# Optimization experiments

Hardware: AMD Instinct MI355X
Metric: run time of the kernel (lower is better)

Reference implementation:

```python
import jax, jax.numpy as jnp
import numpy as np

EPS = 1e-6
NEG_SLOPE = 0.2


def knn_idx(xf, k):
    # xf: (B, C, N) flattened vector features; returns (B, N, k) neighbor indices
    xx = jnp.sum(xf * xf, axis=1)                       # (B, N)
    inner = jnp.einsum('bcn,bcm->bnm', xf, xf)          # (B, N, N)
    neg_dist = 2.0 * inner - xx[:, :, None] - xx[:, None, :]  # -||xi-xj||^2
    _, idx = jax.lax.top_k(neg_dist, k)                 # includes self (dist 0)
    return idx


def get_graph_feature(x, k):
    # x: (B, D, 3, N) -> edge features (B, 2D, 3, N, k)
    B, D, _, N = x.shape
    idx = knn_idx(x.reshape(B, D * 3, N), k)            # (B, N, k)
    pts = jnp.transpose(x, (0, 3, 1, 2))                # (B, N, D, 3)
    neigh = jax.vmap(lambda p, i: p[i])(pts, idx)       # (B, N, k, D, 3) gather
    center = jnp.broadcast_to(pts[:, :, None], neigh.shape)
    feat = jnp.concatenate([neigh - center, center], axis=3)  # (B, N, k, 2D, 3)
    return jnp.transpose(feat, (0, 3, 4, 1, 2))


def vn_linear_leakyrelu(x, Wf, Wd):
    # Vector-Neuron linear + leaky ReLU. x: (B, Cin, 3, ...),
    # Wf: (Cout, Cin), Wd: (Cout, Cin) or (1, Cin) when nonlinearity is shared.
    p = jnp.einsum('oi,bi...->bo...', Wf, x)
    d = jnp.einsum('oi,bi...->bo...', Wd, x)
    dot = jnp.sum(p * d, axis=2, keepdims=True)
    dsq = jnp.sum(d * d, axis=2, keepdims=True)
    proj = p - (dot / (dsq + EPS)) * d
    return NEG_SLOPE * p + (1.0 - NEG_SLOPE) * jnp.where(dot >= 0, p, proj)


def setup_inputs() -> dict:
    key = jax.random.key(0)
    ks = jax.random.split(key, 11)
    B, N = 8, 1024
    x = jax.random.normal(ks[0], (B, 3, N), dtype=jnp.float32)
    # dims = [1, 21, 21, 42, 85, 341]
    ins = [2, 42, 42, 84, 169]      # 2*dim_in for edge layers; sum(dims[1:-1]) for last
    outs = [21, 21, 42, 85, 341]
    dirs = [21, 21, 42, 85, 1]      # last layer has share_nonlinearity=True
    d = {"x": x}
    for i, (ci, co, cd) in enumerate(zip(ins, outs, dirs)):
        s = 1.0 / np.sqrt(ci)
        kf, kd = jax.random.split(ks[1 + i])
        d[f"Wf{i}"] = (jax.random.normal(kf, (co, ci), dtype=jnp.float32) * s)
        d[f"Wd{i}"] = (jax.random.normal(kd, (cd, ci), dtype=jnp.float32) * s)
    d["k"] = 20
    return d


def reference(x, Wf0, Wd0, Wf1, Wd1, Wf2, Wd2, Wf3, Wd3, Wf4, Wd4, k):
    cur = x[:, None]                 # (B, 1, 3, N)
    feats = []
    for Wf, Wd in ((Wf0, Wd0), (Wf1, Wd1), (Wf2, Wd2), (Wf3, Wd3)):
        g = get_graph_feature(cur, k)        # (B, 2D, 3, N, k)
        h = vn_linear_leakyrelu(g, Wf, Wd)   # (B, Dout, 3, N, k)
        cur = h.mean(axis=-1)                # mean over neighbors -> (B, Dout, 3, N)
        feats.append(cur)
    xcat = jnp.concatenate(feats, axis=1)    # (B, 169, 3, N)
    out = vn_linear_leakyrelu(xcat, Wf4, Wd4)
    return out.mean(axis=-1)                 # mean over points -> (B, 341, 3)
```

## Files before the change

kernel.cpp:

```cpp
#include <hip/hip_runtime.h>
#include <cstddef>

#define BB 8
#define NN 1024
#define KK 20
#define CCAT 169
#define NT 16
#define WTLD 384

__global__ __launch_bounds__(256) void dist_tile_kernel(
    const float* __restrict__ src, int bs, int F, float* __restrict__ dist) {
  __shared__ float As[8][128];
  __shared__ float Bs[8][128];
  int b = blockIdx.z;
  int rem = blockIdx.x, bi = 0;
  while (rem >= 8 - bi) { rem -= 8 - bi; ++bi; }
  int bj = bi + rem;
  int n0 = bi * 128;
  int m0 = bj * 128;
  int t = threadIdx.x;
  int tx = t & 15, ty = t >> 4;
  const float* p = src + (size_t)b * bs;

  float acc[8][8];
  float xn[8], xm[8];
#pragma unroll
  for (int i = 0; i < 8; ++i) {
    xn[i] = 0.f;
    xm[i] = 0.f;
#pragma unroll
    for (int j = 0; j < 8; ++j) acc[i][j] = 0.f;
  }

  int fr = t >> 5;
  int cc = (t & 31) << 2;
  for (int f0 = 0; f0 < F; f0 += 8) {
    int f = f0 + fr;
    float4 av = {0.f, 0.f, 0.f, 0.f}, bv = {0.f, 0.f, 0.f, 0.f};
    if (f < F) {
      av = *(const float4*)(p + (size_t)f * NN + n0 + cc);
      bv = *(const float4*)(p + (size_t)f * NN + m0 + cc);
    }
    __syncthreads();
    *(float4*)&As[fr][cc] = av;
    *(float4*)&Bs[fr][cc] = bv;
    __syncthreads();
#pragma unroll
    for (int f2 = 0; f2 < 8; ++f2) {
      float4 al = *(const float4*)&As[f2][ty << 2];
      float4 ah = *(const float4*)&As[f2][64 + (ty << 2)];
      float4 bl = *(const float4*)&Bs[f2][tx << 2];
      float4 bh = *(const float4*)&Bs[f2][64 + (tx << 2)];
      float a[8] = {al.x, al.y, al.z, al.w, ah.x, ah.y, ah.z, ah.w};
      float bb[8] = {bl.x, bl.y, bl.z, bl.w, bh.x, bh.y, bh.z, bh.w};
#pragma unroll
      for (int i = 0; i < 8; ++i) xn[i] += a[i] * a[i];
#pragma unroll
      for (int j = 0; j < 8; ++j) xm[j] += bb[j] * bb[j];
#pragma unroll
      for (int i = 0; i < 8; ++i)
#pragma unroll
        for (int j = 0; j < 8; ++j) acc[i][j] += a[i] * bb[j];
    }
  }

#pragma unroll
  for (int i = 0; i < 8; ++i)
#pragma unroll
    for (int j = 0; j < 8; ++j) acc[i][j] = 2.f * acc[i][j] - xn[i] - xm[j];

#pragma unroll
  for (int i = 0; i < 8; ++i) {
    int n = n0 + ((i < 4) ? ((ty << 2) + i) : (64 + (ty << 2) + i - 4));
    float* dr = dist + (((size_t)b * NN + n) << 10);
    *(float4*)(dr + m0 + (tx << 2)) =
        make_float4(acc[i][0], acc[i][1], acc[i][2], acc[i][3]);
    *(float4*)(dr + m0 + 64 + (tx << 2)) =
        make_float4(acc[i][4], acc[i][5], acc[i][6], acc[i][7]);
  }

  if (bi != bj) {
#pragma unroll
    for (int j = 0; j < 8; ++j) {
      int m = m0 + ((j < 4) ? ((tx << 2) + j) : (64 + (tx << 2) + j - 4));
      float* dr = dist + (((size_t)b * NN + m) << 10);
      *(float4*)(dr + n0 + (ty << 2)) =
          make_float4(acc[0][j], acc[1][j], acc[2][j], acc[3][j]);
      *(float4*)(dr + n0 + 64 + (ty << 2)) =
          make_float4(acc[4][j], acc[5][j], acc[6][j], acc[7][j]);
    }
  }
}

__global__ __launch_bounds__(256) void topk_kernel(
    const float* __restrict__ dist, int* __restrict__ idx_out) {
  int wave = threadIdx.x >> 6;
  int lane = threadIdx.x & 63;
  int row = blockIdx.x * 4 + wave;
  const float* d = dist + ((size_t)row << 10);

  unsigned long long key[16];
  {
    const float4* dp = (const float4*)(d + (lane << 4));
#pragma unroll
    for (int q = 0; q < 4; ++q) {
      float4 v4 = dp[q];
      float vv[4] = {v4.x, v4.y, v4.z, v4.w};
#pragma unroll
      for (int e = 0; e < 4; ++e) {
        int m = (lane << 4) + (q << 2) + e;
        unsigned u = __float_as_uint(vv[e]);
        u = (u & 0x80000000u) ? ~u : (u | 0x80000000u);
        key[(q << 2) + e] =
            ((unsigned long long)u << 32) | (unsigned)(NN - 1 - m);
      }
    }
  }

#pragma unroll
  for (int size = 2; size <= 16; size <<= 1) {
#pragma unroll
    for (int stride = size >> 1; stride > 0; stride >>= 1) {
#pragma unroll
      for (int i = 0; i < 16; ++i) {
        int j = i ^ stride;
        if (j > i) {
          unsigned long long a = key[i], c = key[j];
          bool desc = ((i & size) == 0);
          bool sw = desc ? (a < c) : (a > c);
          key[i] = sw ? c : a;
          key[j] = sw ? a : c;
        }
      }
    }
  }

  int* out = idx_out + row * KK;
  unsigned long long head = key[0];
  for (int r = 0; r < KK; ++r) {
    unsigned hv = (unsigned)(head >> 32);
    unsigned v = hv;
#pragma unroll
    for (int off = 32; off > 0; off >>= 1) {
      unsigned o = __shfl_xor(v, off, 64);
      v = (o > v) ? o : v;
    }
    unsigned long long tie = __ballot(hv == v);
    unsigned il;
    if (tie & (tie - 1)) {
      unsigned c = (hv == v) ? (unsigned)head : 0u;
#pragma unroll
      for (int off = 32; off > 0; off >>= 1) {
        unsigned o = __shfl_xor(c, off, 64);
        c = (o > c) ? o : c;
      }
      il = c;
    } else {
      int wl = __builtin_ctzll(tie);
      il = __shfl((unsigned)head, wl, 64);
    }
    if (lane == 0) out[r] = (NN - 1) - (int)il;
    if (hv == v && (unsigned)head == il) {
#pragma unroll
      for (int s = 0; s < 15; ++s) key[s] = key[s + 1];
      key[15] = 0ull;
      head = key[0];
    }
  }
}

template <int DD>
__global__ __launch_bounds__(256) void edge_fused_kernel(
    const float* __restrict__ src, int bs, int Co, int nsplit,
    const float* __restrict__ Wf, const float* __restrict__ Wd,
    const int* __restrict__ idx, int ooff, float* __restrict__ xcat) {
  __shared__ float2 Ulds[3 * NN];
  __shared__ float2 Vlds[3 * NN];
  __shared__ float4 Wlds[48];
  int bo = blockIdx.x;
  int b = bo / Co, o = bo % Co;
  int t = threadIdx.x;

  if (t < DD) {
    float wfa = Wf[o * 2 * DD + t];
    float wfb = Wf[o * 2 * DD + DD + t] - wfa;
    float wda = Wd[o * 2 * DD + t];
    float wdb = Wd[o * 2 * DD + DD + t] - wda;
    Wlds[t] = make_float4(wfa, wfb, wda, wdb);
  }
  __syncthreads();

  const float* sb = src + (size_t)b * bs;
  {
    int c0 = t << 2;
    float4 uf[3], vf[3], ud[3], vd[3];
#pragma unroll
    for (int r = 0; r < 3; ++r) {
      uf[r] = make_float4(0.f, 0.f, 0.f, 0.f);
      vf[r] = make_float4(0.f, 0.f, 0.f, 0.f);
      ud[r] = make_float4(0.f, 0.f, 0.f, 0.f);
      vd[r] = make_float4(0.f, 0.f, 0.f, 0.f);
    }
#pragma unroll 2
    for (int i = 0; i < DD; ++i) {
      const float* row = sb + (size_t)i * 3 * NN + c0;
      float4 s[3];
      s[0] = *(const float4*)(row);
      s[1] = *(const float4*)(row + 1024);
      s[2] = *(const float4*)(row + 2048);
      float4 w = Wlds[i];
#pragma unroll
      for (int r = 0; r < 3; ++r) {
        uf[r].x += w.x * s[r].x; uf[r].y += w.x * s[r].y;
        uf[r].z += w.x * s[r].z; uf[r].w += w.x * s[r].w;
        vf[r].x += w.y * s[r].x; vf[r].y += w.y * s[r].y;
        vf[r].z += w.y * s[r].z; vf[r].w += w.y * s[r].w;
        ud[r].x += w.z * s[r].x; ud[r].y += w.z * s[r].y;
        ud[r].z += w.z * s[r].z; ud[r].w += w.z * s[r].w;
        vd[r].x += w.w * s[r].x; vd[r].y += w.w * s[r].y;
        vd[r].z += w.w * s[r].z; vd[r].w += w.w * s[r].w;
      }
    }
#pragma unroll
    for (int r = 0; r < 3; ++r) {
      int g = t + 256 * r;
      *(float4*)&Ulds[(g << 2) + 0] =
          make_float4(uf[r].x, ud[r].x, uf[r].y, ud[r].y);
      *(float4*)&Ulds[(g << 2) + 2] =
          make_float4(uf[r].z, ud[r].z, uf[r].w, ud[r].w);
      *(float4*)&Vlds[(g << 2) + 0] =
          make_float4(vf[r].x, vd[r].x, vf[r].y, vd[r].y);
      *(float4*)&Vlds[(g << 2) + 2] =
          make_float4(vf[r].z, vd[r].z, vf[r].w, vd[r].w);
    }
  }
  __syncthreads();

  const float inv_k = 1.f / KK;
  int cnt = NN / nsplit;
  int nbase = blockIdx.y * cnt;
  for (int n = nbase + t; n < nbase + cnt; n += 256) {
    float2 v0 = Vlds[n];
    float2 v1 = Vlds[NN + n];
    float2 v2 = Vlds[2 * NN + n];
    const int4* ip = (const int4*)(idx + (b * NN + n) * KK);
    float a0 = 0.f, a1 = 0.f, a2 = 0.f;
#pragma unroll
    for (int q = 0; q < 5; ++q) {
      int4 iv = ip[q];
      int nbs[4] = {iv.x, iv.y, iv.z, iv.w};
#pragma unroll
      for (int jj = 0; jj < 4; ++jj) {
        int nb = nbs[jj];
        float2 u0 = Ulds[nb];
        float2 u1 = Ulds[NN + nb];
        float2 u2 = Ulds[2 * NN + nb];
        float pf0 = u0.x + v0.x, pd0 = u0.y + v0.y;
        float pf1 = u1.x + v1.x, pd1 = u1.y + v1.y;
        float pf2 = u2.x + v2.x, pd2 = u2.y + v2.y;
        float dot = pf0 * pd0 + pf1 * pd1 + pf2 * pd2;
        float dsq = pd0 * pd0 + pd1 * pd1 + pd2 * pd2;
        float g = (dot >= 0.f) ? 0.f : 0.8f * dot / (dsq + 1e-6f);
        a0 += pf0 - g * pd0;
        a1 += pf1 - g * pd1;
        a2 += pf2 - g * pd2;
      }
    }
    size_t ob = (size_t)b * CCAT * 3 * NN + (size_t)(ooff + o) * 3 * NN + n;
    xcat[ob] = a0 * inv_k;
    xcat[ob + NN] = a1 * inv_k;
    xcat[ob + 2 * NN] = a2 * inv_k;
  }
}

__global__ __launch_bounds__(256) void prep_kernel(
    const float* __restrict__ Wf4, float* __restrict__ Wt,
    float* __restrict__ zpad) {
  int o = blockIdx.x * 256 + threadIdx.x;
  int f = blockIdx.y;
  if (o < WTLD)
    Wt[(size_t)f * WTLD + o] = (f < CCAT && o < 341) ? Wf4[o * CCAT + f] : 0.f;
  if (blockIdx.x == 0 && blockIdx.y == 0) zpad[threadIdx.x] = 0.f;
}

__device__ __forceinline__ void gl2lds16(const float* g, float* l) {
  __builtin_amdgcn_global_load_lds(
      (const __attribute__((address_space(1))) unsigned int*)g,
      (__attribute__((address_space(3))) unsigned int*)l, 16, 0, 0);
}

__global__ __launch_bounds__(256) void final_fused_kernel(
    const float* __restrict__ xcat, const float* __restrict__ Wt,
    const float* __restrict__ Wd4, const float* __restrict__ zpad,
    float* __restrict__ part) {
  __shared__ float Ws[2][16][64];
  __shared__ float Xs[2][3][16][64];
  __shared__ float Wda[176];
  int b = blockIdx.z;
  int o0 = blockIdx.y * 64;
  int n0 = blockIdx.x * 64;
  int t = threadIdx.x;
  int tx = t & 15, ty = t >> 4;

  if (t < 176) Wda[t] = (t < CCAT) ? Wd4[t] : 0.f;

  float acc[3][4][4];
  float dv[3][4];
#pragma unroll
  for (int c = 0; c < 3; ++c) {
#pragma unroll
    for (int i = 0; i < 4; ++i)
#pragma unroll
      for (int j = 0; j < 4; ++j) acc[c][i][j] = 0.f;
#pragma unroll
    for (int j = 0; j < 4; ++j) dv[c][j] = 0.f;
  }

  const float* xb = xcat + (size_t)b * CCAT * 3 * NN;
  const int NTILE = 11;

  {
    const float* wsrc = Wt + (size_t)ty * WTLD + o0 + (tx << 2);
    gl2lds16(wsrc, &Ws[0][ty][tx << 2]);
#pragma unroll
    for (int c = 0; c < 3; ++c) {
      const float* xsrc = xb + ((size_t)ty * 3 + c) * NN + n0 + (tx << 2);
      gl2lds16(xsrc, &Xs[0][c][ty][tx << 2]);
    }
  }

#pragma unroll 1
  for (int tt = 0; tt < NTILE; ++tt) {
    int buf = tt & 1;
    __syncthreads();
    if (tt + 1 < NTILE) {
      int f = (tt + 1) * 16 + ty;
      const float* wsrc = Wt + (size_t)f * WTLD + o0 + (tx << 2);
      gl2lds16(wsrc, &Ws[buf ^ 1][ty][tx << 2]);
#pragma unroll
      for (int c = 0; c < 3; ++c) {
        const float* xsrc = (f < CCAT)
                                ? xb + ((size_t)f * 3 + c) * NN + n0 + (tx << 2)
                                : zpad + (tx << 2);
        gl2lds16(xsrc, &Xs[buf ^ 1][c][ty][tx << 2]);
      }
    }
#pragma unroll
    for (int f2 = 0; f2 < 16; ++f2) {
      float4 w = *(const float4*)&Ws[buf][f2][ty << 2];
      float wa[4] = {w.x, w.y, w.z, w.w};
      float wd = Wda[tt * 16 + f2];
#pragma unroll
      for (int c = 0; c < 3; ++c) {
        float4 x = *(const float4*)&Xs[buf][c][f2][tx << 2];
        float xa[4] = {x.x, x.y, x.z, x.w};
#pragma unroll
        for (int j = 0; j < 4; ++j) dv[c][j] += wd * xa[j];
#pragma unroll
        for (int i = 0; i < 4; ++i)
#pragma unroll
          for (int j = 0; j < 4; ++j) acc[c][i][j] += wa[i] * xa[j];
      }
    }
  }

  float s[3][4];
#pragma unroll
  for (int c = 0; c < 3; ++c)
#pragma unroll
    for (int i = 0; i < 4; ++i) s[c][i] = 0.f;
#pragma unroll
  for (int i = 0; i < 4; ++i) {
#pragma unroll
    for (int j = 0; j < 4; ++j) {
      float d0 = dv[0][j], d1 = dv[1][j], d2 = dv[2][j];
      float p0 = acc[0][i][j], p1 = acc[1][i][j], p2 = acc[2][i][j];
      float dot = p0 * d0 + p1 * d1 + p2 * d2;
      float dsq = d0 * d0 + d1 * d1 + d2 * d2;
      float g = (dot >= 0.f) ? 0.f : 0.8f * dot / (dsq + 1e-6f);
      s[0][i] += p0 - g * d0;
      s[1][i] += p1 - g * d1;
      s[2][i] += p2 - g * d2;
    }
  }

#pragma unroll
  for (int off = 1; off < 16; off <<= 1) {
#pragma unroll
    for (int c = 0; c < 3; ++c)
#pragma unroll
      for (int i = 0; i < 4; ++i) s[c][i] += __shfl_xor(s[c][i], off, 64);
  }
  if (tx == 0) {
#pragma unroll
    for (int i = 0; i < 4; ++i) {
      int o = o0 + (ty << 2) + i;
      if (o < 341) {
#pragma unroll
        for (int c = 0; c < 3; ++c)
          part[(((size_t)b * 341 + o) * 3 + c) * NT + blockIdx.x] = s[c][i];
      }
    }
  }
}

__global__ void final_reduce_kernel(const float* __restrict__ part,
                                    float* __restrict__ out) {
  int t = blockIdx.x * 256 + threadIdx.x;
  if (t >= BB * 341 * 3) return;
  const float* p = part + (size_t)t * NT;
  float s = 0.f;
#pragma unroll
  for (int nt = 0; nt < NT; ++nt) s += p[nt];
  out[t] = s * (1.f / 1024.f);
}

extern "C" void kernel_launch(void* const* d_in, const int* in_sizes, int n_in,
                              void* d_out, int out_size, void* d_ws,
                              size_t ws_size, hipStream_t stream) {
  (void)in_sizes; (void)n_in; (void)out_size; (void)ws_size;
  const float* x = (const float*)d_in[0];
  const float* Wf[5] = {(const float*)d_in[1], (const float*)d_in[3],
                        (const float*)d_in[5], (const float*)d_in[7],
                        (const float*)d_in[9]};
  const float* Wd[5] = {(const float*)d_in[2], (const float*)d_in[4],
                        (const float*)d_in[6], (const float*)d_in[8],
                        (const float*)d_in[10]};

  float* ws = (float*)d_ws;
  float* dist = ws;
  float* part = ws;
  float* Wt = ws + 262144;
  float* zpad = Wt + 176 * WTLD;
  size_t off = (size_t)BB * NN * NN;
  int* idx = (int*)(ws + off);
  off += (size_t)BB * NN * KK;
  float* xcat = ws + off;

  struct LayerCfg { int D, Co, inoff, ooff, nsplit; };
  const LayerCfg L[4] = {
      {1, 21, 0, 0, 4},
      {21, 21, 0, 21, 4},
      {21, 42, 21, 42, 2},
      {42, 85, 42, 84, 1},
  };

  for (int l = 0; l < 4; ++l) {
    const float* src = (l == 0) ? x : (xcat + (size_t)L[l].inoff * 3 * NN);
    int bs = (l == 0) ? 3 * NN : CCAT * 3 * NN;
    int D = L[l].D, Co = L[l].Co;

    dist_tile_kernel<<<dim3(36, 1, BB), 256, 0, stream>>>(src, bs, 3 * D, dist);
    topk_kernel<<<(BB * NN) / 4, 256, 0, stream>>>(dist, idx);
    dim3 eg(BB * Co, L[l].nsplit);
    if (D == 1)
      edge_fused_kernel<1><<<eg, 256, 0, stream>>>(
          src, bs, Co, L[l].nsplit, Wf[l], Wd[l], idx, L[l].ooff, xcat);
    else if (D == 21)
      edge_fused_kernel<21><<<eg, 256, 0, stream>>>(
          src, bs, Co, L[l].nsplit, Wf[l], Wd[l], idx, L[l].ooff, xcat);
    else
      edge_fused_kernel<42><<<eg, 256, 0, stream>>>(
          src, bs, Co, L[l].nsplit, Wf[l], Wd[l], idx, L[l].ooff, xcat);
  }

  prep_kernel<<<dim3(2, 176), 256, 0, stream>>>(Wf[4], Wt, zpad);
  final_fused_kernel<<<dim3(NT, 6, BB), 256, 0, stream>>>(xcat, Wt, Wd[4],
                                                          zpad, part);
  final_reduce_kernel<<<(BB * 341 * 3 + 255) / 256, 256, 0, stream>>>(
      part, (float*)d_out);
}
```

Measured before the change: 426.7 us.

## Double-buffer distance tiles, drop symmetric writes, use LDS queue in top-k

The distance kernel is templated on the feature count and now double-buffers its shared-memory tiles, prefetching the next feature slab while computing the current one. It launches a full 8x8 tile grid instead of exploiting symmetry, so it stops writing transposed tiles at the cost of recomputing the lower triangle. The top-k kernel spills each lane's sorted keys into LDS and pops them through a pointer, replacing the 16-register shift on every pop. This trades more dist FLOPs and extra shared memory for less per-pop register shuffling and fewer strided writes.

```diff
diff --git a/kernel.cpp b/kernel.cpp
--- a/kernel.cpp
+++ b/kernel.cpp
@@ -8,16 +8,14 @@
 #define NT 16
 #define WTLD 384
 
+template <int F>
 __global__ __launch_bounds__(256) void dist_tile_kernel(
-    const float* __restrict__ src, int bs, int F, float* __restrict__ dist) {
-  __shared__ float As[8][128];
-  __shared__ float Bs[8][128];
+    const float* __restrict__ src, int bs, float* __restrict__ dist) {
+  __shared__ float As[2][8][128];
+  __shared__ float Bs[2][8][128];
   int b = blockIdx.z;
-  int rem = blockIdx.x, bi = 0;
-  while (rem >= 8 - bi) { rem -= 8 - bi; ++bi; }
-  int bj = bi + rem;
-  int n0 = bi * 128;
-  int m0 = bj * 128;
+  int n0 = blockIdx.y * 128;
+  int m0 = blockIdx.x * 128;
   int t = threadIdx.x;
   int tx = t & 15, ty = t >> 4;
   const float* p = src + (size_t)b * bs;
@@ -34,23 +32,36 @@
 
   int fr = t >> 5;
   int cc = (t & 31) << 2;
-  for (int f0 = 0; f0 < F; f0 += 8) {
-    int f = f0 + fr;
-    float4 av = {0.f, 0.f, 0.f, 0.f}, bv = {0.f, 0.f, 0.f, 0.f};
-    if (f < F) {
-      av = *(const float4*)(p + (size_t)f * NN + n0 + cc);
-      bv = *(const float4*)(p + (size_t)f * NN + m0 + cc);
-    }
+  constexpr int T = (F + 7) / 8;
+
+  float4 av = {0.f, 0.f, 0.f, 0.f}, bv = {0.f, 0.f, 0.f, 0.f};
+  if (fr < F) {
+    av = *(const float4*)(p + (size_t)fr * NN + n0 + cc);
+    bv = *(const float4*)(p + (size_t)fr * NN + m0 + cc);
+  }
+  *(float4*)&As[0][fr][cc] = av;
+  *(float4*)&Bs[0][fr][cc] = bv;
+
+#pragma unroll 1
+  for (int k = 0; k < T; ++k) {
     __syncthreads();
-    *(float4*)&As[fr][cc] = av;
-    *(float4*)&Bs[fr][cc] = bv;
-    __syncthreads();
+    if (k + 1 < T) {
+      int f = (k + 1) * 8 + fr;
+      av = make_float4(0.f, 0.f, 0.f, 0.f);
+      bv = make_float4(0.f, 0.f, 0.f, 0.f);
+      if (f < F) {
+        av = *(const float4*)(p + (size_t)f * NN + n0 + cc);
+        bv = *(const float4*)(p + (size_t)f * NN + m0 + cc);
+      }
+    }
+    const float(*A)[128] = As[k & 1];
+    const float(*B)[128] = Bs[k & 1];
 #pragma unroll
     for (int f2 = 0; f2 < 8; ++f2) {
-      float4 al = *(const float4*)&As[f2][ty << 2];
-      float4 ah = *(const float4*)&As[f2][64 + (ty << 2)];
-      float4 bl = *(const float4*)&Bs[f2][tx << 2];
-      float4 bh = *(const float4*)&Bs[f2][64 + (tx << 2)];
+      float4 al = *(const float4*)&A[f2][ty << 2];
+      float4 ah = *(const float4*)&A[f2][64 + (ty << 2)];
+      float4 bl = *(const float4*)&B[f2][tx << 2];
+      float4 bh = *(const float4*)&B[f2][64 + (tx << 2)];
       float a[8] = {al.x, al.y, al.z, al.w, ah.x, ah.y, ah.z, ah.w};
       float bb[8] = {bl.x, bl.y, bl.z, bl.w, bh.x, bh.y, bh.z, bh.w};
 #pragma unroll
@@ -61,6 +72,10 @@
       for (int i = 0; i < 8; ++i)
 #pragma unroll
         for (int j = 0; j < 8; ++j) acc[i][j] += a[i] * bb[j];
+    }
+    if (k + 1 < T) {
+      *(float4*)&As[(k + 1) & 1][fr][cc] = av;
+      *(float4*)&Bs[(k + 1) & 1][fr][cc] = bv;
     }
   }
 
@@ -78,22 +93,11 @@
     *(float4*)(dr + m0 + 64 + (tx << 2)) =
         make_float4(acc[i][4], acc[i][5], acc[i][6], acc[i][7]);
   }
-
-  if (bi != bj) {
-#pragma unroll
-    for (int j = 0; j < 8; ++j) {
-      int m = m0 + ((j < 4) ? ((tx << 2) + j) : (64 + (tx << 2) + j - 4));
-      float* dr = dist + (((size_t)b * NN + m) << 10);
-      *(float4*)(dr + n0 + (ty << 2)) =
-          make_float4(acc[0][j], acc[1][j], acc[2][j], acc[3][j]);
-      *(float4*)(dr + n0 + 64 + (ty << 2)) =
-          make_float4(acc[4][j], acc[5][j], acc[6][j], acc[7][j]);
-    }
-  }
 }
 
 __global__ __launch_bounds__(256) void topk_kernel(
     const float* __restrict__ dist, int* __restrict__ idx_out) {
+  __shared__ unsigned long long q[4][16][64];
   int wave = threadIdx.x >> 6;
   int lane = threadIdx.x & 63;
   int row = blockIdx.x * 4 + wave;
@@ -103,15 +107,15 @@
   {
     const float4* dp = (const float4*)(d + (lane << 4));
 #pragma unroll
-    for (int q = 0; q < 4; ++q) {
-      float4 v4 = dp[q];
+    for (int qd = 0; qd < 4; ++qd) {
+      float4 v4 = dp[qd];
       float vv[4] = {v4.x, v4.y, v4.z, v4.w};
 #pragma unroll
       for (int e = 0; e < 4; ++e) {
-        int m = (lane << 4) + (q << 2) + e;
+        int m = (lane << 4) + (qd << 2) + e;
         unsigned u = __float_as_uint(vv[e]);
         u = (u & 0x80000000u) ? ~u : (u | 0x80000000u);
-        key[(q << 2) + e] =
+        key[(qd << 2) + e] =
             ((unsigned long long)u << 32) | (unsigned)(NN - 1 - m);
       }
     }
@@ -135,8 +139,13 @@
     }
   }
 
+#pragma unroll
+  for (int s = 1; s < 16; ++s) q[wave][s - 1][lane] = key[s];
+  q[wave][15][lane] = 0ull;
+
   int* out = idx_out + row * KK;
   unsigned long long head = key[0];
+  int ptr = 0;
   for (int r = 0; r < KK; ++r) {
     unsigned hv = (unsigned)(head >> 32);
     unsigned v = hv;
@@ -161,10 +170,8 @@
     }
     if (lane == 0) out[r] = (NN - 1) - (int)il;
     if (hv == v && (unsigned)head == il) {
-#pragma unroll
-      for (int s = 0; s < 15; ++s) key[s] = key[s + 1];
-      key[15] = 0ull;
-      head = key[0];
+      head = q[wave][ptr][lane];
+      ++ptr;
     }
   }
 }
@@ -246,8 +253,8 @@
     const int4* ip = (const int4*)(idx + (b * NN + n) * KK);
     float a0 = 0.f, a1 = 0.f, a2 = 0.f;
 #pragma unroll
-    for (int q = 0; q < 5; ++q) {
-      int4 iv = ip[q];
+    for (int qq = 0; qq < 5; ++qq) {
+      int4 iv = ip[qq];
       int nbs[4] = {iv.x, iv.y, iv.z, iv.w};
 #pragma unroll
       for (int jj = 0; jj < 4; ++jj) {
@@ -450,8 +457,16 @@
     int bs = (l == 0) ? 3 * NN : CCAT * 3 * NN;
     int D = L[l].D, Co = L[l].Co;
 
-    dist_tile_kernel<<<dim3(36, 1, BB), 256, 0, stream>>>(src, bs, 3 * D, dist);
+    dim3 dg(8, 8, BB);
+    if (D == 1)
+      dist_tile_kernel<3><<<dg, 256, 0, stream>>>(src, bs, dist);
+    else if (D == 21)
+      dist_tile_kernel<63><<<dg, 256, 0, stream>>>(src, bs, dist);
+    else
+      dist_tile_kernel<126><<<dg, 256, 0, stream>>>(src, bs, dist);
+
     topk_kernel<<<(BB * NN) / 4, 256, 0, stream>>>(dist, idx);
+
     dim3 eg(BB * Co, L[l].nsplit);
     if (D == 1)
       edge_fused_kernel<1><<<eg, 256, 0, stream>>>(
```

New measurement: 394.9 us. -7.4%, faster.
